# Performance work log

Hardware: AMD Instinct MI355X
Metric: run time of the kernel (lower is better)

Reference implementation:

```python
import jax, jax.numpy as jnp
import numpy as np

GAMMA = 1.0


def setup_inputs() -> dict:
    key = jax.random.key(0)
    k1, k2, k3 = jax.random.split(key, 3)
    N, D = 65536, 512
    return {
        "anchor": jax.random.normal(k1, (N, D), dtype=jnp.float32),
        "positive": jax.random.normal(k2, (N, D), dtype=jnp.float32),
        "negative": jax.random.normal(k3, (N, D), dtype=jnp.float32),
        "margin": 1,
    }


def reference(anchor, positive, negative, margin):
    m = jnp.asarray(margin, dtype=anchor.dtype)
    delta_p = 1.0 - m
    delta_n = m
    op = 1.0 + m
    on = -m
    # diagonal of anchor @ positive.T == row-wise dot product (same math, O(N*d))
    pos_cos = jnp.sum(anchor * positive, axis=1, keepdims=True)  # [N,1]
    neg_cos = jnp.sum(anchor * negative, axis=1, keepdims=True)  # [N,1]
    alpha_p = jnp.abs(op - pos_cos)
    alpha_n = jnp.abs(neg_cos - on)
    sim_pos = jnp.exp(-GAMMA * alpha_p * (pos_cos - delta_p))
    sim_neg = jnp.exp(GAMMA * alpha_n * (neg_cos - delta_n))
    loss = jnp.log(1.0 + jnp.sum(sim_pos) * jnp.sum(sim_neg))
    return loss
```

## Files before the change

kernel.cpp:

```cpp
#include <hip/hip_runtime.h>
#include <math.h>


#define NEG_BIG (-1.0e30f)

__device__ __forceinline__ float margin_val(const void* p) {
    int iv = *(const int*)p;
    if (iv > -(1 << 23) && iv < (1 << 23)) return (float)iv;
    return *(const float*)p;
}

__device__ __forceinline__ void lse_combine(float& m, float& s, float om, float os) {
    float M = fmaxf(m, om);
    s = s * expf(m - M) + os * expf(om - M);
    m = M;
}

__device__ __forceinline__ void lse_add(float& m, float& s, float a) {
    if (a > m) {
        s = s * expf(m - a) + 1.0f;
        m = a;
    } else {
        s += expf(a - m);
    }
}

__global__ __launch_bounds__(256) void circle_partial(
    const float* __restrict__ anchor,
    const float* __restrict__ positive,
    const float* __restrict__ negative,
    const void* __restrict__ margin_p,
    float4* __restrict__ ws,
    int N)
{
    const float m       = margin_val(margin_p);
    const float delta_p = 1.0f - m;
    const float delta_n = m;
    const float op      = 1.0f + m;
    const float on      = -m;

    const int lane          = threadIdx.x & 63;
    const int wid           = threadIdx.x >> 6;
    const int waves_per_blk = blockDim.x >> 6;
    const int gwave         = blockIdx.x * waves_per_blk + wid;
    const int nwaves        = gridDim.x * waves_per_blk;

    float mp = NEG_BIG, sp = 0.0f;
    float mn = NEG_BIG, sn = 0.0f;

    for (int row = gwave; row < N; row += nwaves) {
        const float4* a4 = (const float4*)(anchor   + (size_t)row * 512);
        const float4* p4 = (const float4*)(positive + (size_t)row * 512);
        const float4* n4 = (const float4*)(negative + (size_t)row * 512);
        float4 a0 = a4[lane], a1 = a4[lane + 64];
        float4 p0 = p4[lane], p1 = p4[lane + 64];
        float4 n0 = n4[lane], n1 = n4[lane + 64];

        float pos = a0.x*p0.x + a0.y*p0.y + a0.z*p0.z + a0.w*p0.w
                  + a1.x*p1.x + a1.y*p1.y + a1.z*p1.z + a1.w*p1.w;
        float neg = a0.x*n0.x + a0.y*n0.y + a0.z*n0.z + a0.w*n0.w
                  + a1.x*n1.x + a1.y*n1.y + a1.z*n1.z + a1.w*n1.w;

        #pragma unroll
        for (int off = 32; off > 0; off >>= 1) {
            pos += __shfl_xor(pos, off, 64);
            neg += __shfl_xor(neg, off, 64);
        }

        float ap = -fabsf(op - pos) * (pos - delta_p);
        float an =  fabsf(neg - on) * (neg - delta_n);
        lse_add(mp, sp, ap);
        lse_add(mn, sn, an);
    }

    __shared__ float s_mp[8], s_sp[8], s_mn[8], s_sn[8];
    if (lane == 0) { s_mp[wid] = mp; s_sp[wid] = sp; s_mn[wid] = mn; s_sn[wid] = sn; }
    __syncthreads();
    if (threadIdx.x == 0) {
        float Mp = NEG_BIG, Sp = 0.0f, Mn = NEG_BIG, Sn = 0.0f;
        for (int i = 0; i < waves_per_blk; ++i) {
            lse_combine(Mp, Sp, s_mp[i], s_sp[i]);
            lse_combine(Mn, Sn, s_mn[i], s_sn[i]);
        }
        ws[blockIdx.x] = make_float4(Mp, Sp, Mn, Sn);
    }
}

__global__ __launch_bounds__(256) void circle_final(
    const float4* __restrict__ ws,
    int nblk,
    float* __restrict__ out)
{
    float mp = NEG_BIG, sp = 0.0f;
    float mn = NEG_BIG, sn = 0.0f;
    for (int i = threadIdx.x; i < nblk; i += blockDim.x) {
        float4 v = ws[i];
        lse_combine(mp, sp, v.x, v.y);
        lse_combine(mn, sn, v.z, v.w);
    }
    #pragma unroll
    for (int off = 32; off > 0; off >>= 1) {
        float omp = __shfl_xor(mp, off, 64);
        float osp = __shfl_xor(sp, off, 64);
        float omn = __shfl_xor(mn, off, 64);
        float osn = __shfl_xor(sn, off, 64);
        lse_combine(mp, sp, omp, osp);
        lse_combine(mn, sn, omn, osn);
    }
    __shared__ float s_mp[4], s_sp[4], s_mn[4], s_sn[4];
    const int lane = threadIdx.x & 63;
    const int wid  = threadIdx.x >> 6;
    if (lane == 0) { s_mp[wid] = mp; s_sp[wid] = sp; s_mn[wid] = mn; s_sn[wid] = sn; }
    __syncthreads();
    if (threadIdx.x == 0) {
        float Mp = NEG_BIG, Sp = 0.0f, Mn = NEG_BIG, Sn = 0.0f;
        for (int i = 0; i < 4; ++i) {
            lse_combine(Mp, Sp, s_mp[i], s_sp[i]);
            lse_combine(Mn, Sn, s_mn[i], s_sn[i]);
        }
        float L = Mp + Mn + logf(Sp) + logf(Sn);
        float loss = fmaxf(L, 0.0f) + log1pf(expf(-fabsf(L)));
        out[0] = loss;
    }
}

extern "C" void kernel_launch(void* const* d_in, const int* in_sizes, int n_in,
                              void* d_out, int out_size, void* d_ws, size_t ws_size,
                              hipStream_t stream) {
    const float* anchor   = (const float*)d_in[0];
    const float* positive = (const float*)d_in[1];
    const float* negative = (const float*)d_in[2];
    const void*  margin   = d_in[3];

    const int N = in_sizes[0] >> 9;

    int nblk = 2048;
    const size_t need = (size_t)nblk * sizeof(float4);
    if (ws_size < need) nblk = (int)(ws_size / sizeof(float4));

    circle_partial<<<nblk, 256, 0, stream>>>(anchor, positive, negative, margin,
                                             (float4*)d_ws, N);
    circle_final<<<1, 256, 0, stream>>>((const float4*)d_ws, nblk, (float*)d_out);
}
```

Before: 80.79 us.

## Process eight rows per wavefront with 8-lane groups and shorter shuffle reductions

Each wavefront now splits into eight groups of eight lanes, with each group handling one row through a 16-iteration float4 loop. Only three shuffle steps are needed per row instead of six. A cross-group log-sum-exp merge runs once after the loop. This cuts shuffle and per-row reduction overhead and puts more loads in flight per lane, but the access pattern now spans eight rows per wavefront with 32 contiguous floats per group, which may affect coalescing. It also assumes 256-thread blocks.

```diff
diff --git a/kernel.cpp b/kernel.cpp
--- a/kernel.cpp
+++ b/kernel.cpp
@@ -16,15 +16,6 @@
     m = M;
 }
 
-__device__ __forceinline__ void lse_add(float& m, float& s, float a) {
-    if (a > m) {
-        s = s * expf(m - a) + 1.0f;
-        m = a;
-    } else {
-        s += expf(a - m);
-    }
-}
-
 __global__ __launch_bounds__(256) void circle_partial(
     const float* __restrict__ anchor,
     const float* __restrict__ positive,
@@ -39,46 +30,64 @@
     const float op      = 1.0f + m;
     const float on      = -m;
 
-    const int lane          = threadIdx.x & 63;
-    const int wid           = threadIdx.x >> 6;
-    const int waves_per_blk = blockDim.x >> 6;
-    const int gwave         = blockIdx.x * waves_per_blk + wid;
-    const int nwaves        = gridDim.x * waves_per_blk;
+    const int lane  = threadIdx.x & 63;
+    const int wid   = threadIdx.x >> 6;
+    const int g     = lane >> 3;
+    const int c     = lane & 7;
+    const int gwave = blockIdx.x * 4 + wid;
+    const int nwaves = gridDim.x * 4;
 
     float mp = NEG_BIG, sp = 0.0f;
     float mn = NEG_BIG, sn = 0.0f;
 
-    for (int row = gwave; row < N; row += nwaves) {
-        const float4* a4 = (const float4*)(anchor   + (size_t)row * 512);
-        const float4* p4 = (const float4*)(positive + (size_t)row * 512);
-        const float4* n4 = (const float4*)(negative + (size_t)row * 512);
-        float4 a0 = a4[lane], a1 = a4[lane + 64];
-        float4 p0 = p4[lane], p1 = p4[lane + 64];
-        float4 n0 = n4[lane], n1 = n4[lane + 64];
+    const int nbatch = (N + 7) >> 3;
+    for (int b = gwave; b < nbatch; b += nwaves) {
+        const int row   = b * 8 + g;
+        const bool valid = (row < N);
 
-        float pos = a0.x*p0.x + a0.y*p0.y + a0.z*p0.z + a0.w*p0.w
-                  + a1.x*p1.x + a1.y*p1.y + a1.z*p1.z + a1.w*p1.w;
-        float neg = a0.x*n0.x + a0.y*n0.y + a0.z*n0.z + a0.w*n0.w
-                  + a1.x*n1.x + a1.y*n1.y + a1.z*n1.z + a1.w*n1.w;
+        float pos = 0.0f, neg = 0.0f;
+        if (valid) {
+            const float4* a4 = (const float4*)(anchor   + (size_t)row * 512);
+            const float4* p4 = (const float4*)(positive + (size_t)row * 512);
+            const float4* n4 = (const float4*)(negative + (size_t)row * 512);
+            #pragma unroll 4
+            for (int k = 0; k < 16; ++k) {
+                float4 a = a4[c + 8 * k];
+                float4 p = p4[c + 8 * k];
+                float4 n = n4[c + 8 * k];
+                pos += a.x*p.x + a.y*p.y + a.z*p.z + a.w*p.w;
+                neg += a.x*n.x + a.y*n.y + a.z*n.z + a.w*n.w;
+            }
+        }
 
         #pragma unroll
-        for (int off = 32; off > 0; off >>= 1) {
+        for (int off = 1; off < 8; off <<= 1) {
             pos += __shfl_xor(pos, off, 64);
             neg += __shfl_xor(neg, off, 64);
         }
 
-        float ap = -fabsf(op - pos) * (pos - delta_p);
-        float an =  fabsf(neg - on) * (neg - delta_n);
-        lse_add(mp, sp, ap);
-        lse_add(mn, sn, an);
+        float ap = valid ? -fabsf(op - pos) * (pos - delta_p) : NEG_BIG;
+        float an = valid ?  fabsf(neg - on) * (neg - delta_n) : NEG_BIG;
+        lse_combine(mp, sp, ap, valid ? 1.0f : 0.0f);
+        lse_combine(mn, sn, an, valid ? 1.0f : 0.0f);
     }
 
-    __shared__ float s_mp[8], s_sp[8], s_mn[8], s_sn[8];
+    #pragma unroll
+    for (int off = 8; off < 64; off <<= 1) {
+        float omp = __shfl_xor(mp, off, 64);
+        float osp = __shfl_xor(sp, off, 64);
+        float omn = __shfl_xor(mn, off, 64);
+        float osn = __shfl_xor(sn, off, 64);
+        lse_combine(mp, sp, omp, osp);
+        lse_combine(mn, sn, omn, osn);
+    }
+
+    __shared__ float s_mp[4], s_sp[4], s_mn[4], s_sn[4];
     if (lane == 0) { s_mp[wid] = mp; s_sp[wid] = sp; s_mn[wid] = mn; s_sn[wid] = sn; }
     __syncthreads();
     if (threadIdx.x == 0) {
         float Mp = NEG_BIG, Sp = 0.0f, Mn = NEG_BIG, Sn = 0.0f;
-        for (int i = 0; i < waves_per_blk; ++i) {
+        for (int i = 0; i < 4; ++i) {
             lse_combine(Mp, Sp, s_mp[i], s_sp[i]);
             lse_combine(Mn, Sn, s_mn[i], s_sn[i]);
         }
```

New measurement: 81.57 us. No clear change (+1.0%).
